# Performance work log

Hardware: AMD Instinct MI355X
Metric: run time of the kernel (lower is better)

## Reference

```python
import jax, jax.numpy as jnp
import numpy as np

TOP_K = 4


def setup_inputs() -> dict:
    key = jax.random.key(0)
    k1, k2, k3 = jax.random.split(key, 3)
    T, H, E = 16384, 2880, 128
    hidden_states = jax.random.normal(k1, (T, H), dtype=jnp.float32)
    weight = jax.random.normal(k2, (E, H), dtype=jnp.float32) * 0.02
    bias = jax.random.normal(k3, (E,), dtype=jnp.float32) * 0.02
    return {"hidden_states": hidden_states, "weight": weight, "bias": bias}


def reference(hidden_states, weight, bias):
    # [T, H] @ [H, E] + [E] -> router logits [T, E]
    hidden_states = hidden_states.reshape(-1, weight.shape[1])
    router_logits = jnp.einsum('th,eh->te', hidden_states, weight) + bias
    # top-k over experts, then softmax over the k selected logits
    router_top_value, router_indices = jax.lax.top_k(router_logits, TOP_K)
    router_scores = jax.nn.softmax(router_top_value, axis=-1)
    return router_scores, router_indices
```

## Files before the change

### kernel.cpp

```cpp
#include <hip/hip_runtime.h>
#include <hip/hip_bf16.h>
#include <math.h>

#define T_TOKENS 16384
#define H_DIM    2880
#define KHALF    1440
#define E_EXP    128
#define TOPK     4
#define MT       32
#define KC       32
#define NCHUNK   (H_DIM / KC)
#define NCHUNK_H (KHALF / KC)
#define EPS_GAP  5e-4f

#define WS_WOFF   64
#define WS_WBYTES (NCHUNK * 1024 * 16)
#define WS_FLOFF  (WS_WOFF + WS_WBYTES)
#define WS_NEED   (WS_FLOFF + T_TOKENS * 4)

typedef __bf16 bf16x8 __attribute__((ext_vector_type(8)));
typedef float  f32x4  __attribute__((ext_vector_type(4)));

__device__ __forceinline__ void split2(float a, float b,
                                       unsigned int& hi, unsigned int& lo) {
    float2 p; p.x = a; p.y = b;
    __hip_bfloat162 h = __float22bfloat162_rn(p);
    unsigned int hu; __builtin_memcpy(&hu, &h, 4);
    float2 r;
    r.x = a - __uint_as_float((hu & 0xffffu) << 16);
    r.y = b - __uint_as_float(hu & 0xffff0000u);
    __hip_bfloat162 l = __float22bfloat162_rn(r);
    unsigned int lu; __builtin_memcpy(&lu, &l, 4);
    hi = hu; lo = lu;
}

__global__ __launch_bounds__(256) void prep_w(const float* __restrict__ W,
                                              uint4* __restrict__ wsW) {
    const int f   = blockIdx.x * 256 + threadIdx.x;
    const int kc  = f >> 9;
    const int rem = f & 511;
    const int nt  = rem >> 6;
    const int L   = rem & 63;
    const int e   = nt * 16 + (L & 15);
    const int k   = kc * KC + (L >> 4) * 8;
    const float* p = W + (size_t)e * H_DIM + k;
    const float4 x0 = *(const float4*)p;
    const float4 x1 = *(const float4*)(p + 4);
    uint4 hi, lo;
    split2(x0.x, x0.y, hi.x, lo.x);
    split2(x0.z, x0.w, hi.y, lo.y);
    split2(x1.x, x1.y, hi.z, lo.z);
    split2(x1.z, x1.w, hi.w, lo.w);
    wsW[(size_t)kc * 1024 + nt * 64 + L]       = hi;
    wsW[(size_t)kc * 1024 + 512 + nt * 64 + L] = lo;
}

__global__ __launch_bounds__(512, 4) void router_main(
    const float* __restrict__ A, const uint4* __restrict__ wsW,
    const float* __restrict__ bias, float* __restrict__ out,
    int* __restrict__ flag_count, int* __restrict__ flag_list)
{
    __shared__ __align__(16) uint2 sAhi[2][2][128];
    __shared__ __align__(16) uint2 sAlo[2][2][128];
    __shared__ __align__(16) uint4 sW[2][1024];
    __shared__ float sL[MT][129];

    const int tid    = threadIdx.x;
    const int t_base = blockIdx.x * MT;

    const int wave  = tid >> 6;
    const int L     = tid & 63;
    const int whalf = wave >> 2;
    const int wm    = wave & 1;
    const int wn    = (wave >> 1) & 1;

    const int shalf = tid >> 8;
    const int tid_h = tid & 255;
    const int at = tid_h >> 3;
    const int ac = tid_h & 7;
    const int a_idx = (at >> 4) * 128 + ((((ac >> 1) << 4) | (at & 15)) << 1) + (ac & 1);
    const float* Ag = A + (size_t)(t_base + at) * H_DIM + shalf * KHALF + ac * 4;

    const int wv = (wave & 3);
    const uint4* wsrc = wsW + (size_t)(shalf * NCHUNK_H) * 1024 + (wv * 4) * 64 + L;

    uint2* sAhiF = &sAhi[shalf][0][0];
    uint2* sAloF = &sAlo[shalf][0][0];

    f32x4 acc[4];
#pragma unroll
    for (int i = 0; i < 4; ++i) { f32x4 z = {0.f, 0.f, 0.f, 0.f}; acc[i] = z; }

    float4 av = *(const float4*)Ag;

    for (int it = 0; it < NCHUNK_H; ++it) {
        uint2 ahp, alp;
        split2(av.x, av.y, ahp.x, alp.x);
        split2(av.z, av.w, ahp.y, alp.y);

        __syncthreads();

        sAhiF[a_idx] = ahp;
        sAloF[a_idx] = alp;

        const uint4* wc = wsrc + (size_t)it * 1024;
#pragma unroll
        for (int j = 0; j < 4; ++j) {
            __builtin_amdgcn_global_load_lds(
                (const __attribute__((address_space(1))) void*)(wc + j * 64),
                (__attribute__((address_space(3))) void*)&sW[shalf][(wv * 4 + j) * 64],
                16, 0, 0);
        }

        __syncthreads();

        if (it + 1 < NCHUNK_H) av = *(const float4*)(Ag + (it + 1) * KC);

        const bf16x8 ahi = *(const bf16x8*)&sAhi[whalf][wm][L * 2];
        const bf16x8 alo = *(const bf16x8*)&sAlo[whalf][wm][L * 2];
#pragma unroll
        for (int i = 0; i < 4; ++i) {
            const int nt = wn * 4 + i;
            const bf16x8 whi = *(const bf16x8*)&sW[whalf][nt * 64 + L];
            const bf16x8 wlo = *(const bf16x8*)&sW[whalf][512 + nt * 64 + L];
            acc[i] = __builtin_amdgcn_mfma_f32_16x16x32_bf16(ahi, whi, acc[i], 0, 0, 0);
            acc[i] = __builtin_amdgcn_mfma_f32_16x16x32_bf16(ahi, wlo, acc[i], 0, 0, 0);
            acc[i] = __builtin_amdgcn_mfma_f32_16x16x32_bf16(alo, whi, acc[i], 0, 0, 0);
        }
    }

    __syncthreads();
    if (whalf == 0) {
#pragma unroll
        for (int i = 0; i < 4; ++i) {
            const int e = wn * 64 + i * 16 + (L & 15);
            const float b = bias[e];
#pragma unroll
            for (int r = 0; r < 4; ++r)
                sL[wm * 16 + (L >> 4) * 4 + r][e] = acc[i][r] + b;
        }
    }
    __syncthreads();
    if (whalf == 1) {
#pragma unroll
        for (int i = 0; i < 4; ++i) {
            const int e = wn * 64 + i * 16 + (L & 15);
#pragma unroll
            for (int r = 0; r < 4; ++r)
                sL[wm * 16 + (L >> 4) * 4 + r][e] += acc[i][r];
        }
    }
    __syncthreads();

    if (tid < MT) {
        float v0 = -1e30f, v1 = -1e30f, v2 = -1e30f, v3 = -1e30f, v4 = -1e30f;
        int   i0 = 0, i1 = 0, i2 = 0, i3 = 0, i4 = 0;
        for (int e = 0; e < E_EXP; ++e) {
            const float x = sL[tid][e];
            if (x > v4) {
                if (x > v0)      { v4=v3;i4=i3; v3=v2;i3=i2; v2=v1;i2=i1; v1=v0;i1=i0; v0=x;i0=e; }
                else if (x > v1) { v4=v3;i4=i3; v3=v2;i3=i2; v2=v1;i2=i1; v1=x;i1=e; }
                else if (x > v2) { v4=v3;i4=i3; v3=v2;i3=i2; v2=x;i2=e; }
                else if (x > v3) { v4=v3;i4=i3; v3=x;i3=e; }
                else             { v4=x;i4=e; }
            }
        }
        const float g0 = v0 - v1, g1 = v1 - v2, g2 = v2 - v3, g3 = v3 - v4;
        float mg = g0 < g1 ? g0 : g1;
        mg = mg < g2 ? mg : g2;
        mg = mg < g3 ? mg : g3;

        const float e0x = expf(v0 - v0);
        const float e1x = expf(v1 - v0);
        const float e2x = expf(v2 - v0);
        const float e3x = expf(v3 - v0);
        const float s   = e0x + e1x + e2x + e3x;

        const int gt = t_base + tid;
        float* out_scores = out;
        float* out_idx    = out + (size_t)T_TOKENS * TOPK;
        out_scores[gt * 4 + 0] = e0x / s;
        out_scores[gt * 4 + 1] = e1x / s;
        out_scores[gt * 4 + 2] = e2x / s;
        out_scores[gt * 4 + 3] = e3x / s;
        out_idx[gt * 4 + 0] = (float)i0;
        out_idx[gt * 4 + 1] = (float)i1;
        out_idx[gt * 4 + 2] = (float)i2;
        out_idx[gt * 4 + 3] = (float)i3;

        if (mg < EPS_GAP) {
            const int p = atomicAdd(flag_count, 1);
            if (p < T_TOKENS) flag_list[p] = gt;
        }
    }
}

__global__ __launch_bounds__(512, 4) void router_main_fb(
    const float* __restrict__ A, const float* __restrict__ W,
    const float* __restrict__ bias, float* __restrict__ out,
    int* __restrict__ flag_count, int* __restrict__ flag_list)
{
    __shared__ __align__(16) uint2 sAhi[2][2][128];
    __shared__ __align__(16) uint2 sAlo[2][2][128];
    __shared__ __align__(16) uint4 sWhi[2][8][64];
    __shared__ __align__(16) uint4 sWlo[2][8][64];
    __shared__ float sL[MT][129];

    const int tid    = threadIdx.x;
    const int t_base = blockIdx.x * MT;
    const int wave  = tid >> 6;
    const int L     = tid & 63;
    const int whalf = wave >> 2;
    const int wm    = wave & 1;
    const int wn    = (wave >> 1) & 1;
    const int shalf = tid >> 8;
    const int tid_h = tid & 255;
    const int at = tid_h >> 3;
    const int ac = tid_h & 7;
    const int a_idx = (at >> 4) * 128 + ((((ac >> 1) << 4) | (at & 15)) << 1) + (ac & 1);
    const float* Ag = A + (size_t)(t_base + at) * H_DIM + shalf * KHALF + ac * 4;
    const int we  = tid_h >> 1;
    const int wq0 = (tid_h & 1) * 2;
    const float* Wg = W + (size_t)we * H_DIM + shalf * KHALF + wq0 * 8;
    const int w_nt = we >> 4;
    const int w_n  = we & 15;

    uint2* sAhiF = &sAhi[shalf][0][0];
    uint2* sAloF = &sAlo[shalf][0][0];

    f32x4 acc[4];
#pragma unroll
    for (int i = 0; i < 4; ++i) { f32x4 z = {0.f, 0.f, 0.f, 0.f}; acc[i] = z; }

    for (int k0 = 0; k0 < KHALF; k0 += KC) {
        const float4 av  = *(const float4*)(Ag + k0);
        const float4 wv0 = *(const float4*)(Wg + k0);
        const float4 wv1 = *(const float4*)(Wg + k0 + 4);
        const float4 wv2 = *(const float4*)(Wg + k0 + 8);
        const float4 wv3 = *(const float4*)(Wg + k0 + 12);

        uint2 ahp, alp;
        split2(av.x, av.y, ahp.x, alp.x);
        split2(av.z, av.w, ahp.y, alp.y);
        uint4 whp0, wlp0, whp1, wlp1;
        split2(wv0.x, wv0.y, whp0.x, wlp0.x);
        split2(wv0.z, wv0.w, whp0.y, wlp0.y);
        split2(wv1.x, wv1.y, whp0.z, wlp0.z);
        split2(wv1.z, wv1.w, whp0.w, wlp0.w);
        split2(wv2.x, wv2.y, whp1.x, wlp1.x);
        split2(wv2.z, wv2.w, whp1.y, wlp1.y);
        split2(wv3.x, wv3.y, whp1.z, wlp1.z);
        split2(wv3.z, wv3.w, whp1.w, wlp1.w);

        __syncthreads();
        sAhiF[a_idx] = ahp;
        sAloF[a_idx] = alp;
        sWhi[shalf][w_nt][((wq0 + 0) << 4) | w_n] = whp0;
        sWhi[shalf][w_nt][((wq0 + 1) << 4) | w_n] = whp1;
        sWlo[shalf][w_nt][((wq0 + 0) << 4) | w_n] = wlp0;
        sWlo[shalf][w_nt][((wq0 + 1) << 4) | w_n] = wlp1;
        __syncthreads();

        const bf16x8 ahi = *(const bf16x8*)&sAhi[whalf][wm][L * 2];
        const bf16x8 alo = *(const bf16x8*)&sAlo[whalf][wm][L * 2];
#pragma unroll
        for (int i = 0; i < 4; ++i) {
            const int nt = wn * 4 + i;
            const bf16x8 whi = *(const bf16x8*)&sWhi[whalf][nt][L];
            const bf16x8 wlo = *(const bf16x8*)&sWlo[whalf][nt][L];
            acc[i] = __builtin_amdgcn_mfma_f32_16x16x32_bf16(ahi, whi, acc[i], 0, 0, 0);
            acc[i] = __builtin_amdgcn_mfma_f32_16x16x32_bf16(ahi, wlo, acc[i], 0, 0, 0);
            acc[i] = __builtin_amdgcn_mfma_f32_16x16x32_bf16(alo, whi, acc[i], 0, 0, 0);
        }
    }

    __syncthreads();
    if (whalf == 0) {
#pragma unroll
        for (int i = 0; i < 4; ++i) {
            const int e = wn * 64 + i * 16 + (L & 15);
            const float b = bias[e];
#pragma unroll
            for (int r = 0; r < 4; ++r)
                sL[wm * 16 + (L >> 4) * 4 + r][e] = acc[i][r] + b;
        }
    }
    __syncthreads();
    if (whalf == 1) {
#pragma unroll
        for (int i = 0; i < 4; ++i) {
            const int e = wn * 64 + i * 16 + (L & 15);
#pragma unroll
            for (int r = 0; r < 4; ++r)
                sL[wm * 16 + (L >> 4) * 4 + r][e] += acc[i][r];
        }
    }
    __syncthreads();

    if (tid < MT) {
        float v0 = -1e30f, v1 = -1e30f, v2 = -1e30f, v3 = -1e30f, v4 = -1e30f;
        int   i0 = 0, i1 = 0, i2 = 0, i3 = 0, i4 = 0;
        for (int e = 0; e < E_EXP; ++e) {
            const float x = sL[tid][e];
            if (x > v4) {
                if (x > v0)      { v4=v3;i4=i3; v3=v2;i3=i2; v2=v1;i2=i1; v1=v0;i1=i0; v0=x;i0=e; }
                else if (x > v1) { v4=v3;i4=i3; v3=v2;i3=i2; v2=v1;i2=i1; v1=x;i1=e; }
                else if (x > v2) { v4=v3;i4=i3; v3=v2;i3=i2; v2=x;i2=e; }
                else if (x > v3) { v4=v3;i4=i3; v3=x;i3=e; }
                else             { v4=x;i4=e; }
            }
        }
        const float g0 = v0 - v1, g1 = v1 - v2, g2 = v2 - v3, g3 = v3 - v4;
        float mg = g0 < g1 ? g0 : g1;
        mg = mg < g2 ? mg : g2;
        mg = mg < g3 ? mg : g3;

        const float e0x = expf(v0 - v0);
        const float e1x = expf(v1 - v0);
        const float e2x = expf(v2 - v0);
        const float e3x = expf(v3 - v0);
        const float s   = e0x + e1x + e2x + e3x;

        const int gt = t_base + tid;
        float* out_scores = out;
        float* out_idx    = out + (size_t)T_TOKENS * TOPK;
        out_scores[gt * 4 + 0] = e0x / s;
        out_scores[gt * 4 + 1] = e1x / s;
        out_scores[gt * 4 + 2] = e2x / s;
        out_scores[gt * 4 + 3] = e3x / s;
        out_idx[gt * 4 + 0] = (float)i0;
        out_idx[gt * 4 + 1] = (float)i1;
        out_idx[gt * 4 + 2] = (float)i2;
        out_idx[gt * 4 + 3] = (float)i3;

        if (mg < EPS_GAP) {
            const int p = atomicAdd(flag_count, 1);
            if (p < T_TOKENS) flag_list[p] = gt;
        }
    }
}

__global__ __launch_bounds__(256) void router_recheck(
    const float* __restrict__ A, const float* __restrict__ W,
    const float* __restrict__ bias, float* __restrict__ out,
    const int* __restrict__ flag_count, const int* __restrict__ flag_list)
{
    __shared__ double sPart[256];
    __shared__ double sLog[E_EXP];

    int count = *flag_count;
    if (count > T_TOKENS) count = T_TOKENS;

    const int tid = threadIdx.x;
    const int e   = tid & (E_EXP - 1);
    const int h   = tid >> 7;

    for (int i = blockIdx.x; i < count; i += gridDim.x) {
        const int t = flag_list[i];
        const float* arow = A + (size_t)t * H_DIM + h * KHALF;
        const float* wrow = W + (size_t)e * H_DIM + h * KHALF;

        double s0 = 0.0, s1 = 0.0, s2 = 0.0, s3 = 0.0;
        float4 a[8], w[8];
#pragma unroll
        for (int q = 0; q < 8; ++q) {
            a[q] = *(const float4*)(arow + q * 4);
            w[q] = *(const float4*)(wrow + q * 4);
        }
        for (int it = 0; it < KHALF / 32 - 1; ++it) {
            const float* ap = arow + (it + 1) * 32;
            const float* wp = wrow + (it + 1) * 32;
            float4 na[8], nw[8];
#pragma unroll
            for (int q = 0; q < 8; ++q) {
                na[q] = *(const float4*)(ap + q * 4);
                nw[q] = *(const float4*)(wp + q * 4);
            }
#pragma unroll
            for (int q = 0; q < 8; ++q) {
                s0 += (double)a[q].x * (double)w[q].x;
                s1 += (double)a[q].y * (double)w[q].y;
                s2 += (double)a[q].z * (double)w[q].z;
                s3 += (double)a[q].w * (double)w[q].w;
            }
#pragma unroll
            for (int q = 0; q < 8; ++q) { a[q] = na[q]; w[q] = nw[q]; }
        }
#pragma unroll
        for (int q = 0; q < 8; ++q) {
            s0 += (double)a[q].x * (double)w[q].x;
            s1 += (double)a[q].y * (double)w[q].y;
            s2 += (double)a[q].z * (double)w[q].z;
            s3 += (double)a[q].w * (double)w[q].w;
        }
        sPart[tid] = (s0 + s1) + (s2 + s3);
        __syncthreads();
        if (h == 0) sLog[e] = sPart[e] + sPart[e + 128] + (double)bias[e];
        __syncthreads();

        if (tid == 0) {
            double v0 = -1e300, v1 = -1e300, v2 = -1e300, v3 = -1e300;
            int    i0 = 0, i1 = 0, i2 = 0, i3 = 0;
            for (int q = 0; q < E_EXP; ++q) {
                const double x = sLog[q];
                if (x > v3) {
                    if (x > v0)      { v3=v2;i3=i2; v2=v1;i2=i1; v1=v0;i1=i0; v0=x;i0=q; }
                    else if (x > v1) { v3=v2;i3=i2; v2=v1;i2=i1; v1=x;i1=q; }
                    else if (x > v2) { v3=v2;i3=i2; v2=x;i2=q; }
                    else             { v3=x;i3=q; }
                }
            }
            const double e0x = exp(v0 - v0);
            const double e1x = exp(v1 - v0);
            const double e2x = exp(v2 - v0);
            const double e3x = exp(v3 - v0);
            const double s   = e0x + e1x + e2x + e3x;
            float* out_scores = out;
            float* out_idx    = out + (size_t)T_TOKENS * TOPK;
            out_scores[t * 4 + 0] = (float)(e0x / s);
            out_scores[t * 4 + 1] = (float)(e1x / s);
            out_scores[t * 4 + 2] = (float)(e2x / s);
            out_scores[t * 4 + 3] = (float)(e3x / s);
            out_idx[t * 4 + 0] = (float)i0;
            out_idx[t * 4 + 1] = (float)i1;
            out_idx[t * 4 + 2] = (float)i2;
            out_idx[t * 4 + 3] = (float)i3;
        }
        __syncthreads();
    }
}

extern "C" void kernel_launch(void* const* d_in, const int* in_sizes, int n_in,
                              void* d_out, int out_size, void* d_ws, size_t ws_size,
                              hipStream_t stream) {
    const float* A    = (const float*)d_in[0];
    const float* W    = (const float*)d_in[1];
    const float* bias = (const float*)d_in[2];
    float* out = (float*)d_out;

    if (ws_size >= (size_t)WS_NEED) {
        int*  flag_count = (int*)d_ws;
        int*  flag_list  = (int*)((char*)d_ws + WS_FLOFF);
        uint4* wsW       = (uint4*)((char*)d_ws + WS_WOFF);
        hipMemsetAsync(flag_count, 0, sizeof(int), stream);
        prep_w<<<dim3((NCHUNK * 512) / 256), dim3(256), 0, stream>>>(W, wsW);
        router_main<<<dim3(T_TOKENS / MT), dim3(512), 0, stream>>>(A, wsW, bias, out,
                                                                   flag_count, flag_list);
        router_recheck<<<dim3(512), dim3(256), 0, stream>>>(A, W, bias, out,
                                                            flag_count, flag_list);
    } else {
        int* flag_count = (int*)d_ws;
        int* flag_list  = (int*)d_ws + 1;
        hipMemsetAsync(flag_count, 0, sizeof(int), stream);
        router_main_fb<<<dim3(T_TOKENS / MT), dim3(512), 0, stream>>>(A, W, bias, out,
                                                                      flag_count, flag_list);
        router_recheck<<<dim3(512), dim3(256), 0, stream>>>(A, W, bias, out,
                                                            flag_count, flag_list);
    }
}
```

Before: 386.6 us.

## Switch router GEMM to 32x32x16 MFMA with 4-way K split and double buffering

Restructures the main router kernel so that each pair of waves handles one quarter of the K dimension using 32x32x16 bf16 MFMAs, replacing the 16x16x32 tiles over two K halves. The weight prep layout is changed to match the new fragments. Shared-memory A and W staging is double-buffered, with one barrier per iteration instead of two. Partial logits are reduced through two shared arrays that reuse the staging memory via a union. This is meant to improve MFMA efficiency and overlap loads with compute, at the cost of a more complex reduction and more accumulator registers.

```diff
diff --git a/kernel.cpp b/kernel.cpp
--- a/kernel.cpp
+++ b/kernel.cpp
@@ -9,17 +9,19 @@
 #define TOPK     4
 #define MT       32
 #define KC       32
-#define NCHUNK   (H_DIM / KC)
-#define NCHUNK_H (KHALF / KC)
+#define KQ       720
+#define NIT      45
+#define NC16     180
 #define EPS_GAP  5e-4f
 
 #define WS_WOFF   64
-#define WS_WBYTES (NCHUNK * 1024 * 16)
+#define WS_WBYTES (NC16 * 512 * 16)
 #define WS_FLOFF  (WS_WOFF + WS_WBYTES)
 #define WS_NEED   (WS_FLOFF + T_TOKENS * 4)
 
 typedef __bf16 bf16x8 __attribute__((ext_vector_type(8)));
 typedef float  f32x4  __attribute__((ext_vector_type(4)));
+typedef float  f32x16 __attribute__((ext_vector_type(16)));
 
 __device__ __forceinline__ void split2(float a, float b,
                                        unsigned int& hi, unsigned int& lo) {
@@ -37,12 +39,14 @@
 __global__ __launch_bounds__(256) void prep_w(const float* __restrict__ W,
                                               uint4* __restrict__ wsW) {
     const int f   = blockIdx.x * 256 + threadIdx.x;
-    const int kc  = f >> 9;
-    const int rem = f & 511;
-    const int nt  = rem >> 6;
-    const int L   = rem & 63;
-    const int e   = nt * 16 + (L & 15);
-    const int k   = kc * KC + (L >> 4) * 8;
+    const int c16 = f >> 8;
+    const int rem = f & 255;
+    const int nf  = rem >> 6;
+    const int kg  = (rem >> 5) & 1;
+    const int e5  = rem & 31;
+    const int e   = nf * 32 + e5;
+    const int k   = c16 * 16 + kg * 8;
+    const int L   = kg * 32 + e5;
     const float* p = W + (size_t)e * H_DIM + k;
     const float4 x0 = *(const float4*)p;
     const float4 x1 = *(const float4*)(p + 4);
@@ -51,8 +55,8 @@
     split2(x0.z, x0.w, hi.y, lo.y);
     split2(x1.x, x1.y, hi.z, lo.z);
     split2(x1.z, x1.w, hi.w, lo.w);
-    wsW[(size_t)kc * 1024 + nt * 64 + L]       = hi;
-    wsW[(size_t)kc * 1024 + 512 + nt * 64 + L] = lo;
+    wsW[(size_t)c16 * 512 + (nf * 2 + 0) * 64 + L] = hi;
+    wsW[(size_t)c16 * 512 + (nf * 2 + 1) * 64 + L] = lo;
 }
 
 __global__ __launch_bounds__(512, 4) void router_main(
@@ -60,94 +64,109 @@
     const float* __restrict__ bias, float* __restrict__ out,
     int* __restrict__ flag_count, int* __restrict__ flag_list)
 {
-    __shared__ __align__(16) uint2 sAhi[2][2][128];
-    __shared__ __align__(16) uint2 sAlo[2][2][128];
-    __shared__ __align__(16) uint4 sW[2][1024];
-    __shared__ float sL[MT][129];
+    union SMem {
+        struct {
+            uint4 W [2][4][8][64];
+            uint4 Af[2][4][2][64];
+        } s;
+        struct {
+            float L0[MT][129];
+            float L1[MT][129];
+        } r;
+    };
+    __shared__ SMem sm;
 
     const int tid    = threadIdx.x;
     const int t_base = blockIdx.x * MT;
-
-    const int wave  = tid >> 6;
-    const int L     = tid & 63;
-    const int whalf = wave >> 2;
-    const int wm    = wave & 1;
-    const int wn    = (wave >> 1) & 1;
-
-    const int shalf = tid >> 8;
-    const int tid_h = tid & 255;
-    const int at = tid_h >> 3;
-    const int ac = tid_h & 7;
-    const int a_idx = (at >> 4) * 128 + ((((ac >> 1) << 4) | (at & 15)) << 1) + (ac & 1);
-    const float* Ag = A + (size_t)(t_base + at) * H_DIM + shalf * KHALF + ac * 4;
-
-    const int wv = (wave & 3);
-    const uint4* wsrc = wsW + (size_t)(shalf * NCHUNK_H) * 1024 + (wv * 4) * 64 + L;
-
-    uint2* sAhiF = &sAhi[shalf][0][0];
-    uint2* sAloF = &sAlo[shalf][0][0];
-
-    f32x4 acc[4];
-#pragma unroll
-    for (int i = 0; i < 4; ++i) { f32x4 z = {0.f, 0.f, 0.f, 0.f}; acc[i] = z; }
-
-    float4 av = *(const float4*)Ag;
-
-    for (int it = 0; it < NCHUNK_H; ++it) {
-        uint2 ahp, alp;
-        split2(av.x, av.y, ahp.x, alp.x);
-        split2(av.z, av.w, ahp.y, alp.y);
-
-        __syncthreads();
-
-        sAhiF[a_idx] = ahp;
-        sAloF[a_idx] = alp;
-
-        const uint4* wc = wsrc + (size_t)it * 1024;
-#pragma unroll
-        for (int j = 0; j < 4; ++j) {
-            __builtin_amdgcn_global_load_lds(
-                (const __attribute__((address_space(1))) void*)(wc + j * 64),
-                (__attribute__((address_space(3))) void*)&sW[shalf][(wv * 4 + j) * 64],
-                16, 0, 0);
-        }
-
-        __syncthreads();
-
-        if (it + 1 < NCHUNK_H) av = *(const float4*)(Ag + (it + 1) * KC);
-
-        const bf16x8 ahi = *(const bf16x8*)&sAhi[whalf][wm][L * 2];
-        const bf16x8 alo = *(const bf16x8*)&sAlo[whalf][wm][L * 2];
-#pragma unroll
-        for (int i = 0; i < 4; ++i) {
-            const int nt = wn * 4 + i;
-            const bf16x8 whi = *(const bf16x8*)&sW[whalf][nt * 64 + L];
-            const bf16x8 wlo = *(const bf16x8*)&sW[whalf][512 + nt * 64 + L];
-            acc[i] = __builtin_amdgcn_mfma_f32_16x16x32_bf16(ahi, whi, acc[i], 0, 0, 0);
-            acc[i] = __builtin_amdgcn_mfma_f32_16x16x32_bf16(ahi, wlo, acc[i], 0, 0, 0);
-            acc[i] = __builtin_amdgcn_mfma_f32_16x16x32_bf16(alo, whi, acc[i], 0, 0, 0);
-        }
-    }
-
-    __syncthreads();
-    if (whalf == 0) {
-#pragma unroll
-        for (int i = 0; i < 4; ++i) {
-            const int e = wn * 64 + i * 16 + (L & 15);
-            const float b = bias[e];
-#pragma unroll
-            for (int r = 0; r < 4; ++r)
-                sL[wm * 16 + (L >> 4) * 4 + r][e] = acc[i][r] + b;
-        }
-    }
-    __syncthreads();
-    if (whalf == 1) {
-#pragma unroll
-        for (int i = 0; i < 4; ++i) {
-            const int e = wn * 64 + i * 16 + (L & 15);
-#pragma unroll
-            for (int r = 0; r < 4; ++r)
-                sL[wm * 16 + (L >> 4) * 4 + r][e] += acc[i][r];
+    const int wave = tid >> 6;
+    const int l    = tid & 63;
+    const int q    = wave >> 1;
+    const int half = wave & 1;
+    const int tok  = l & 31;
+    const int kg   = l >> 5;
+
+    const float* Ag = A + (size_t)(t_base + tok) * H_DIM + q * KQ + kg * 8;
+    const uint4* wsrc = wsW + (size_t)q * (NIT * 512) + (half * 4) * 64 + l;
+
+    f32x16 acc[2];
+#pragma unroll
+    for (int i = 0; i < 2; ++i)
+#pragma unroll
+        for (int r = 0; r < 16; ++r) acc[i][r] = 0.0f;
+
+#define STAGE_AW(NB, IT1)                                                      \
+    {                                                                          \
+        uint4 hi4, lo4;                                                        \
+        split2(av0.x, av0.y, hi4.x, lo4.x);                                    \
+        split2(av0.z, av0.w, hi4.y, lo4.y);                                    \
+        split2(av1.x, av1.y, hi4.z, lo4.z);                                    \
+        split2(av1.z, av1.w, hi4.w, lo4.w);                                    \
+        sm.s.Af[NB][q][half][l] = half ? lo4 : hi4;                            \
+        const uint4* wc = wsrc + (size_t)(IT1) * 512;                          \
+        _Pragma("unroll")                                                      \
+        for (int j = 0; j < 4; ++j) {                                          \
+            __builtin_amdgcn_global_load_lds(                                  \
+                (const __attribute__((address_space(1))) void*)(wc + j * 64),  \
+                (__attribute__((address_space(3))) void*)&sm.s.W[NB][q][half * 4 + j][0], \
+                16, 0, 0);                                                     \
+        }                                                                      \
+    }
+
+    float4 av0 = *(const float4*)(Ag);
+    float4 av1 = *(const float4*)(Ag + 4);
+    STAGE_AW(0, 0);
+    av0 = *(const float4*)(Ag + 16);
+    av1 = *(const float4*)(Ag + 20);
+    __syncthreads();
+
+    int b = 0;
+    for (int it = 0; it < NIT; ++it) {
+        if (it + 1 < NIT) {
+            STAGE_AW(b ^ 1, it + 1);
+            if (it + 2 < NIT) {
+                av0 = *(const float4*)(Ag + (it + 2) * 16);
+                av1 = *(const float4*)(Ag + (it + 2) * 16 + 4);
+            }
+        }
+        const bf16x8 ahi = *(const bf16x8*)&sm.s.Af[b][q][0][l];
+        const bf16x8 alo = *(const bf16x8*)&sm.s.Af[b][q][1][l];
+#pragma unroll
+        for (int n = 0; n < 2; ++n) {
+            const int fr = (half * 2 + n) * 2;
+            const bf16x8 whi = *(const bf16x8*)&sm.s.W[b][q][fr][l];
+            const bf16x8 wlo = *(const bf16x8*)&sm.s.W[b][q][fr + 1][l];
+            acc[n] = __builtin_amdgcn_mfma_f32_32x32x16_bf16(ahi, whi, acc[n], 0, 0, 0);
+            acc[n] = __builtin_amdgcn_mfma_f32_32x32x16_bf16(ahi, wlo, acc[n], 0, 0, 0);
+            acc[n] = __builtin_amdgcn_mfma_f32_32x32x16_bf16(alo, whi, acc[n], 0, 0, 0);
+        }
+        __syncthreads();
+        b ^= 1;
+    }
+
+    if (q == 0 || q == 2) {
+        float (*Ld)[129] = (q == 0) ? sm.r.L0 : sm.r.L1;
+#pragma unroll
+        for (int n = 0; n < 2; ++n) {
+            const int e = half * 64 + n * 32 + (l & 31);
+            const float bv = (q == 0) ? bias[e] : 0.0f;
+#pragma unroll
+            for (int r = 0; r < 16; ++r) {
+                const int trow = (r & 3) + 8 * (r >> 2) + 4 * (l >> 5);
+                Ld[trow][e] = acc[n][r] + bv;
+            }
+        }
+    }
+    __syncthreads();
+    if (q == 1 || q == 3) {
+        float (*Ld)[129] = (q == 1) ? sm.r.L0 : sm.r.L1;
+#pragma unroll
+        for (int n = 0; n < 2; ++n) {
+            const int e = half * 64 + n * 32 + (l & 31);
+#pragma unroll
+            for (int r = 0; r < 16; ++r) {
+                const int trow = (r & 3) + 8 * (r >> 2) + 4 * (l >> 5);
+                Ld[trow][e] += acc[n][r];
+            }
         }
     }
     __syncthreads();
@@ -156,7 +175,7 @@
         float v0 = -1e30f, v1 = -1e30f, v2 = -1e30f, v3 = -1e30f, v4 = -1e30f;
         int   i0 = 0, i1 = 0, i2 = 0, i3 = 0, i4 = 0;
         for (int e = 0; e < E_EXP; ++e) {
-            const float x = sL[tid][e];
+            const float x = sm.r.L0[tid][e] + sm.r.L1[tid][e];
             if (x > v4) {
                 if (x > v0)      { v4=v3;i4=i3; v3=v2;i3=i2; v2=v1;i2=i1; v1=v0;i1=i0; v0=x;i0=e; }
                 else if (x > v1) { v4=v3;i4=i3; v3=v2;i3=i2; v2=v1;i2=i1; v1=x;i1=e; }
@@ -193,6 +212,7 @@
             if (p < T_TOKENS) flag_list[p] = gt;
         }
     }
+#undef STAGE_AW
 }
 
 __global__ __launch_bounds__(512, 4) void router_main_fb(
@@ -443,7 +463,7 @@
         int*  flag_list  = (int*)((char*)d_ws + WS_FLOFF);
         uint4* wsW       = (uint4*)((char*)d_ws + WS_WOFF);
         hipMemsetAsync(flag_count, 0, sizeof(int), stream);
-        prep_w<<<dim3((NCHUNK * 512) / 256), dim3(256), 0, stream>>>(W, wsW);
+        prep_w<<<dim3(NC16), dim3(256), 0, stream>>>(W, wsW);
         router_main<<<dim3(T_TOKENS / MT), dim3(512), 0, stream>>>(A, wsW, bias, out,
                                                                    flag_count, flag_list);
         router_recheck<<<dim3(512), dim3(256), 0, stream>>>(A, W, bias, out,
```

New measurement: 483.1 us. 1.25x slower.

## Double-buffer LDS stages so loads overlap MFMA with one barrier per chunk

Applied to the files above, without the earlier changes.

Converts the K loop to a double-buffered pipeline: the next chunk's A split and W global_load_lds go into the alternate LDS buffer while MFMAs consume the current one, cutting the syncs per iteration from two to one. Only the first 256 threads now load A, each handling 8 floats, and the logits buffer shares LDS with the staging buffers through a union to limit LDS growth. The cost is more LDS per block, which may lower occupancy against the launch bound of 4 blocks. It also relies on the asynchronous LDS writes having completed by the single barrier.

```diff
diff --git a/kernel.cpp b/kernel.cpp
--- a/kernel.cpp
+++ b/kernel.cpp
@@ -60,10 +60,15 @@
     const float* __restrict__ bias, float* __restrict__ out,
     int* __restrict__ flag_count, int* __restrict__ flag_list)
 {
-    __shared__ __align__(16) uint2 sAhi[2][2][128];
-    __shared__ __align__(16) uint2 sAlo[2][2][128];
-    __shared__ __align__(16) uint4 sW[2][1024];
-    __shared__ float sL[MT][129];
+    union SMem {
+        struct {
+            uint4 W  [2][2][1024];
+            uint4 Ahi[2][2][2][64];
+            uint4 Alo[2][2][2][64];
+        } s;
+        float L[MT][129];
+    };
+    __shared__ SMem sm;
 
     const int tid    = threadIdx.x;
     const int t_base = blockIdx.x * MT;
@@ -75,69 +80,82 @@
     const int wn    = (wave >> 1) & 1;
 
     const int shalf = tid >> 8;
-    const int tid_h = tid & 255;
-    const int at = tid_h >> 3;
-    const int ac = tid_h & 7;
-    const int a_idx = (at >> 4) * 128 + ((((ac >> 1) << 4) | (at & 15)) << 1) + (ac & 1);
-    const float* Ag = A + (size_t)(t_base + at) * H_DIM + shalf * KHALF + ac * 4;
-
-    const int wv = (wave & 3);
+    const int wv    = wave & 3;
     const uint4* wsrc = wsW + (size_t)(shalf * NCHUNK_H) * 1024 + (wv * 4) * 64 + L;
 
-    uint2* sAhiF = &sAhi[shalf][0][0];
-    uint2* sAloF = &sAlo[shalf][0][0];
+    const bool doA = tid < 256;
+    const int at   = tid & 31;
+    const int ac   = (tid >> 5) & 7;
+    const int ah   = ac >> 2;
+    const int akq  = ac & 3;
+    const int awm  = at >> 4;
+    const int aL   = (akq << 4) | (at & 15);
+    const float* Ag = A + (size_t)(t_base + at) * H_DIM + ah * KHALF + akq * 8;
 
     f32x4 acc[4];
 #pragma unroll
     for (int i = 0; i < 4; ++i) { f32x4 z = {0.f, 0.f, 0.f, 0.f}; acc[i] = z; }
 
-    float4 av = *(const float4*)Ag;
-
+#define STAGE(NB, IT)                                                          \
+    {                                                                          \
+        if (doA) {                                                             \
+            uint4 hi4, lo4;                                                    \
+            split2(av0.x, av0.y, hi4.x, lo4.x);                                \
+            split2(av0.z, av0.w, hi4.y, lo4.y);                                \
+            split2(av1.x, av1.y, hi4.z, lo4.z);                                \
+            split2(av1.z, av1.w, hi4.w, lo4.w);                                \
+            sm.s.Ahi[NB][ah][awm][aL] = hi4;                                   \
+            sm.s.Alo[NB][ah][awm][aL] = lo4;                                   \
+        }                                                                      \
+        const uint4* wc = wsrc + (size_t)(IT) * 1024;                          \
+        _Pragma("unroll")                                                      \
+        for (int j = 0; j < 4; ++j) {                                          \
+            __builtin_amdgcn_global_load_lds(                                  \
+                (const __attribute__((address_space(1))) void*)(wc + j * 64),  \
+                (__attribute__((address_space(3))) void*)&sm.s.W[NB][shalf][(wv * 4 + j) * 64], \
+                16, 0, 0);                                                     \
+        }                                                                      \
+    }
+
+    float4 av0, av1;
+    if (doA) { av0 = *(const float4*)(Ag); av1 = *(const float4*)(Ag + 4); }
+    STAGE(0, 0);
+    if (doA) { av0 = *(const float4*)(Ag + KC); av1 = *(const float4*)(Ag + KC + 4); }
+    __syncthreads();
+
+    int b = 0;
     for (int it = 0; it < NCHUNK_H; ++it) {
-        uint2 ahp, alp;
-        split2(av.x, av.y, ahp.x, alp.x);
-        split2(av.z, av.w, ahp.y, alp.y);
-
-        __syncthreads();
-
-        sAhiF[a_idx] = ahp;
-        sAloF[a_idx] = alp;
-
-        const uint4* wc = wsrc + (size_t)it * 1024;
-#pragma unroll
-        for (int j = 0; j < 4; ++j) {
-            __builtin_amdgcn_global_load_lds(
-                (const __attribute__((address_space(1))) void*)(wc + j * 64),
-                (__attribute__((address_space(3))) void*)&sW[shalf][(wv * 4 + j) * 64],
-                16, 0, 0);
-        }
-
-        __syncthreads();
-
-        if (it + 1 < NCHUNK_H) av = *(const float4*)(Ag + (it + 1) * KC);
-
-        const bf16x8 ahi = *(const bf16x8*)&sAhi[whalf][wm][L * 2];
-        const bf16x8 alo = *(const bf16x8*)&sAlo[whalf][wm][L * 2];
+        if (it + 1 < NCHUNK_H) {
+            STAGE(b ^ 1, it + 1);
+            if (doA && it + 2 < NCHUNK_H) {
+                av0 = *(const float4*)(Ag + (it + 2) * KC);
+                av1 = *(const float4*)(Ag + (it + 2) * KC + 4);
+            }
+        }
+        const bf16x8 ahi = *(const bf16x8*)&sm.s.Ahi[b][whalf][wm][L];
+        const bf16x8 alo = *(const bf16x8*)&sm.s.Alo[b][whalf][wm][L];
 #pragma unroll
         for (int i = 0; i < 4; ++i) {
             const int nt = wn * 4 + i;
-            const bf16x8 whi = *(const bf16x8*)&sW[whalf][nt * 64 + L];
-            const bf16x8 wlo = *(const bf16x8*)&sW[whalf][512 + nt * 64 + L];
+            const bf16x8 whi = *(const bf16x8*)&sm.s.W[b][whalf][nt * 64 + L];
+            const bf16x8 wlo = *(const bf16x8*)&sm.s.W[b][whalf][512 + nt * 64 + L];
             acc[i] = __builtin_amdgcn_mfma_f32_16x16x32_bf16(ahi, whi, acc[i], 0, 0, 0);
             acc[i] = __builtin_amdgcn_mfma_f32_16x16x32_bf16(ahi, wlo, acc[i], 0, 0, 0);
             acc[i] = __builtin_amdgcn_mfma_f32_16x16x32_bf16(alo, whi, acc[i], 0, 0, 0);
         }
-    }
-
-    __syncthreads();
+        __syncthreads();
+        b ^= 1;
+    }
+#undef STAGE
+
     if (whalf == 0) {
 #pragma unroll
         for (int i = 0; i < 4; ++i) {
             const int e = wn * 64 + i * 16 + (L & 15);
-            const float b = bias[e];
+            const float bv = bias[e];
 #pragma unroll
             for (int r = 0; r < 4; ++r)
-                sL[wm * 16 + (L >> 4) * 4 + r][e] = acc[i][r] + b;
+                sm.L[wm * 16 + (L >> 4) * 4 + r][e] = acc[i][r] + bv;
         }
     }
     __syncthreads();
@@ -147,7 +165,7 @@
             const int e = wn * 64 + i * 16 + (L & 15);
 #pragma unroll
             for (int r = 0; r < 4; ++r)
-                sL[wm * 16 + (L >> 4) * 4 + r][e] += acc[i][r];
+                sm.L[wm * 16 + (L >> 4) * 4 + r][e] += acc[i][r];
         }
     }
     __syncthreads();
@@ -156,7 +174,7 @@
         float v0 = -1e30f, v1 = -1e30f, v2 = -1e30f, v3 = -1e30f, v4 = -1e30f;
         int   i0 = 0, i1 = 0, i2 = 0, i3 = 0, i4 = 0;
         for (int e = 0; e < E_EXP; ++e) {
-            const float x = sL[tid][e];
+            const float x = sm.L[tid][e];
             if (x > v4) {
                 if (x > v0)      { v4=v3;i4=i3; v3=v2;i3=i2; v2=v1;i2=i1; v1=v0;i1=i0; v0=x;i0=e; }
                 else if (x > v1) { v4=v3;i4=i3; v3=v2;i3=i2; v2=v1;i2=i1; v1=x;i1=e; }
```

Result: no change. 379.7 us (-1.8%).
